# Performance work log

Measured on AMD Instinct MI355X. Metric: run time of the kernel, lower is better.

The kernel has to match this reference:

```python
import jax, jax.numpy as jnp
import numpy as np

N_S, N_T, E, B = 100000, 100000, 2000000, 10000
F_XS, F_XT, F_E, F_U = 10, 5, 10, 10


def setup_inputs() -> dict:
    key = jax.random.key(0)
    ks = jax.random.split(key, 8)
    return {
        "x_s": jax.random.normal(ks[0], (N_S, F_XS), dtype=jnp.float32),
        "x_t": jax.random.normal(ks[1], (N_T, F_XT), dtype=jnp.float32),
        "edge_index": jax.random.randint(ks[2], (2, E), 0, N_S),
        "edge_attr": jax.random.normal(ks[3], (E, F_E), dtype=jnp.float32),
        "u": jax.random.normal(ks[4], (B, F_U), dtype=jnp.float32),
        "batch_e": jax.random.randint(ks[5], (E,), 0, B),
        "W1": jax.random.normal(ks[6], (F_XS + F_XT + F_E + F_U, F_E), dtype=jnp.float32) * (1.0 / np.sqrt(F_XS + F_XT + F_E + F_U)),
        "b1": jnp.zeros((F_E,), dtype=jnp.float32),
        "W2": jax.random.normal(ks[7], (F_E, F_E), dtype=jnp.float32) * (1.0 / np.sqrt(F_E)),
        "b2": jnp.zeros((F_E,), dtype=jnp.float32),
    }


def reference(x_s, x_t, edge_index, edge_attr, u, batch_e, W1, b1, W2, b2):
    src, tgt = edge_index[0], edge_index[1]
    # Gather + concat: [E, F_xs + F_xt + F_e + F_u]
    h = jnp.concatenate([x_s[src], x_t[tgt], edge_attr, u[batch_e]], axis=-1)
    h = jax.nn.leaky_relu(h @ W1 + b1, negative_slope=0.1)
    return h @ W2 + b2  # [E, F_e]
```

## Files before the change

### kernel.cpp

```cpp
#include <hip/hip_runtime.h>


#define F_XS 10
#define F_XT 5
#define F_E  10
#define F_U  10
#define F_IN 35
#define BLOCK 256

typedef float vf4 __attribute__((ext_vector_type(4)));
typedef float vf2 __attribute__((ext_vector_type(2)));
typedef int   vi4 __attribute__((ext_vector_type(4)));
typedef _Float16 f16;

__global__ __launch_bounds__(256) void convert_tables_kernel(
    const float* __restrict__ xs, const float* __restrict__ xt, const float* __restrict__ uu,
    f16* __restrict__ xs_h, f16* __restrict__ xt_h, f16* __restrict__ u_h,
    int n_xs_elems, int n_u_elems, int n_t_rows)
{
    const int tid = blockIdx.x * blockDim.x + threadIdx.x;
    if (tid < n_xs_elems) {
        xs_h[tid] = (f16)xs[tid];
    } else if (tid < n_xs_elems + n_u_elems) {
        const int i = tid - n_xs_elems;
        u_h[i] = (f16)uu[i];
    } else {
        const int r = tid - n_xs_elems - n_u_elems;
        if (r < n_t_rows) {
            const float* p = xt + (long long)r * F_XT;
            f16* q = xt_h + (long long)r * 6;
            #pragma unroll
            for (int i = 0; i < 5; ++i) q[i] = (f16)p[i];
            q[5] = (f16)0.f;
        }
    }
}

__device__ __forceinline__ void compute_edge_attrfirst(
    const f16* __restrict__ s, const f16* __restrict__ t, const f16* __restrict__ uv,
    const float* __restrict__ a,
    const float* __restrict__ W1, const float* __restrict__ b1,
    const float* __restrict__ W2, const float* __restrict__ b2,
    float* __restrict__ o)
{
    float h[F_E];
    #pragma unroll
    for (int j = 0; j < F_E; ++j) h[j] = b1[j];

    #pragma unroll
    for (int k = 0; k < 10; ++k) {
        const float x = a[k];
        #pragma unroll
        for (int j = 0; j < F_E; ++j) h[j] = fmaf(x, W1[(15 + k) * F_E + j], h[j]);
    }
    #pragma unroll
    for (int k = 0; k < 10; ++k) {
        const float x = (float)s[k];
        #pragma unroll
        for (int j = 0; j < F_E; ++j) h[j] = fmaf(x, W1[k * F_E + j], h[j]);
    }
    #pragma unroll
    for (int k = 0; k < 5; ++k) {
        const float x = (float)t[k];
        #pragma unroll
        for (int j = 0; j < F_E; ++j) h[j] = fmaf(x, W1[(10 + k) * F_E + j], h[j]);
    }
    #pragma unroll
    for (int k = 0; k < 10; ++k) {
        const float x = (float)uv[k];
        #pragma unroll
        for (int j = 0; j < F_E; ++j) h[j] = fmaf(x, W1[(25 + k) * F_E + j], h[j]);
    }

    #pragma unroll
    for (int j = 0; j < F_E; ++j) h[j] = (h[j] >= 0.0f) ? h[j] : 0.1f * h[j];

    #pragma unroll
    for (int j = 0; j < F_E; ++j) o[j] = b2[j];
    #pragma unroll
    for (int k = 0; k < F_E; ++k) {
        const float x = h[k];
        #pragma unroll
        for (int j = 0; j < F_E; ++j) o[j] = fmaf(x, W2[k * F_E + j], o[j]);
    }
}

__global__ __launch_bounds__(256, 8) void edge_model_lds2_kernel(
    const f16*   __restrict__ xs_h,
    const f16*   __restrict__ xt_h,
    const int*   __restrict__ edge_index,
    const float* __restrict__ edge_attr,
    const f16*   __restrict__ u_h,
    const int*   __restrict__ batch_e,
    const float* __restrict__ W1,
    const float* __restrict__ b1,
    const float* __restrict__ W2,
    const float* __restrict__ b2,
    float*       __restrict__ out,
    int E)
{
    __shared__ __align__(16) int   idx_lds[3 * BLOCK];
    __shared__ __align__(16) float row_lds[10 * BLOCK];

    const int tid = threadIdx.x;
    const long long blockBase = (long long)blockIdx.x * BLOCK;

    if (blockBase + BLOCK <= E) {
        vi4 idxv;
        if (tid < 192) {
            const int* p;
            if (tid < 64)       p = edge_index + blockBase + 4 * tid;
            else if (tid < 128) p = edge_index + E + blockBase + 4 * (tid - 64);
            else                p = batch_e + blockBase + 4 * (tid - 128);
            idxv = __builtin_nontemporal_load((const vi4*)p);
        }

        const vf4* pa = (const vf4*)(edge_attr + blockBase * F_E);
        vf4 A0 = __builtin_nontemporal_load(pa + tid);
        vf4 A1 = __builtin_nontemporal_load(pa + tid + 256);
        vf4 A2;
        if (tid < 128) A2 = __builtin_nontemporal_load(pa + tid + 512);

        if (tid < 192) *(vi4*)(idx_lds + 4 * tid) = idxv;
        *(vf4*)(row_lds + 4 * tid)         = A0;
        *(vf4*)(row_lds + 4 * (tid + 256)) = A1;
        if (tid < 128) *(vf4*)(row_lds + 4 * (tid + 512)) = A2;
        __syncthreads();

        const int src = idx_lds[tid];
        const int tgt = idx_lds[256 + tid];
        const int be  = idx_lds[512 + tid];

        f16 s[10];  __builtin_memcpy(s,  xs_h + (long long)src * 10, 20);
        f16 tt[8];  __builtin_memcpy(tt, xt_h + (long long)tgt * 6, 16);
        f16 uv[10]; __builtin_memcpy(uv, u_h  + (long long)be  * 10, 20);

        float af[F_E];
        #pragma unroll
        for (int q = 0; q < 5; ++q) {
            const vf2 v = *(const vf2*)(row_lds + 10 * tid + 2 * q);
            af[2 * q]     = v.x;
            af[2 * q + 1] = v.y;
        }

        float o[F_E];
        compute_edge_attrfirst(s, tt, uv, af, W1, b1, W2, b2, o);

        #pragma unroll
        for (int q = 0; q < 5; ++q) {
            vf2 v; v.x = o[2 * q]; v.y = o[2 * q + 1];
            *(vf2*)(row_lds + 10 * tid + 2 * q) = v;
        }
        __syncthreads();

        float* po = out + blockBase * F_E;
        *(vf4*)(po + 4 * tid)         = *(const vf4*)(row_lds + 4 * tid);
        *(vf4*)(po + 4 * (tid + 256)) = *(const vf4*)(row_lds + 4 * (tid + 256));
        if (tid < 128)
            *(vf4*)(po + 4 * (tid + 512)) = *(const vf4*)(row_lds + 4 * (tid + 512));
    } else {
        const long long e = blockBase + tid;
        if (e < E) {
            const int src = edge_index[e];
            const int tgt = edge_index[E + e];
            const int be  = batch_e[e];
            f16 s1[10], t1[8], u1[10];
            __builtin_memcpy(s1, xs_h + (long long)src * 10, 20);
            __builtin_memcpy(t1, xt_h + (long long)tgt * 6, 16);
            __builtin_memcpy(u1, u_h  + (long long)be  * 10, 20);
            float a1[F_E];
            #pragma unroll
            for (int k = 0; k < F_E; ++k) a1[k] = edge_attr[e * F_E + k];
            float o1[F_E];
            compute_edge_attrfirst(s1, t1, u1, a1, W1, b1, W2, b2, o1);
            #pragma unroll
            for (int j = 0; j < F_E; ++j) out[e * F_E + j] = o1[j];
        }
    }
}

__global__ __launch_bounds__(256) void edge_model_f16tab_kernel(
    const f16*   __restrict__ xs_h, const f16* __restrict__ xt_h,
    const int*   __restrict__ edge_index, const float* __restrict__ edge_attr,
    const f16*   __restrict__ u_h, const int* __restrict__ batch_e,
    const float* __restrict__ W1, const float* __restrict__ b1,
    const float* __restrict__ W2, const float* __restrict__ b2,
    float* __restrict__ out, int E)
{
    const int e = blockIdx.x * blockDim.x + threadIdx.x;
    if (e >= E) return;

    const int src = __builtin_nontemporal_load(edge_index + e);
    const int tgt = __builtin_nontemporal_load(edge_index + E + e);
    const int be  = __builtin_nontemporal_load(batch_e + e);

    f16 s[10];  __builtin_memcpy(s, xs_h + (long long)src * 10, 20);
    f16 t[8];   __builtin_memcpy(t, xt_h + (long long)tgt * 6, 16);
    f16 uv[10]; __builtin_memcpy(uv, u_h + (long long)be * 10, 20);

    const float* pe = edge_attr + (long long)e * F_E;
    vf4 a0 = __builtin_nontemporal_load((const vf4*)(pe));
    vf4 a1 = __builtin_nontemporal_load((const vf4*)(pe + 4));
    vf2 a2 = __builtin_nontemporal_load((const vf2*)(pe + 8));
    float af[F_E] = {a0.x,a0.y,a0.z,a0.w, a1.x,a1.y,a1.z,a1.w, a2.x,a2.y};

    float o[F_E];
    compute_edge_attrfirst(s, t, uv, af, W1, b1, W2, b2, o);

    float* po = out + (long long)e * F_E;
    vf4 w0; w0.x=o[0]; w0.y=o[1]; w0.z=o[2]; w0.w=o[3];
    vf4 w1; w1.x=o[4]; w1.y=o[5]; w1.z=o[6]; w1.w=o[7];
    vf2 w2; w2.x=o[8]; w2.y=o[9];
    *(vf4*)(po)     = w0;
    *(vf4*)(po + 4) = w1;
    *(vf2*)(po + 8) = w2;
}

__global__ __launch_bounds__(256) void edge_model_f32_kernel(
    const float* __restrict__ x_s, const float* __restrict__ x_t,
    const int*   __restrict__ edge_index, const float* __restrict__ edge_attr,
    const float* __restrict__ u, const int* __restrict__ batch_e,
    const float* __restrict__ W1, const float* __restrict__ b1,
    const float* __restrict__ W2, const float* __restrict__ b2,
    float* __restrict__ out, int E)
{
    const int e = blockIdx.x * blockDim.x + threadIdx.x;
    if (e >= E) return;
    const int src = __builtin_nontemporal_load(edge_index + e);
    const int tgt = __builtin_nontemporal_load(edge_index + E + e);
    const int be  = __builtin_nontemporal_load(batch_e + e);

    float in[F_IN];
    __builtin_memcpy(in,      x_s + (long long)src * F_XS, 40);
    __builtin_memcpy(in + 10, x_t + (long long)tgt * F_XT, 20);
    const float* pe = edge_attr + (long long)e * F_E;
    vf4 a0 = __builtin_nontemporal_load((const vf4*)(pe));
    vf4 a1 = __builtin_nontemporal_load((const vf4*)(pe + 4));
    vf2 a2 = __builtin_nontemporal_load((const vf2*)(pe + 8));
    in[15]=a0.x; in[16]=a0.y; in[17]=a0.z; in[18]=a0.w;
    in[19]=a1.x; in[20]=a1.y; in[21]=a1.z; in[22]=a1.w;
    in[23]=a2.x; in[24]=a2.y;
    __builtin_memcpy(in + 25, u + (long long)be * F_U, 40);

    float h[F_E];
    #pragma unroll
    for (int j = 0; j < F_E; ++j) h[j] = b1[j];
    #pragma unroll
    for (int k = 0; k < F_IN; ++k) {
        const float a = in[k];
        #pragma unroll
        for (int j = 0; j < F_E; ++j) h[j] = fmaf(a, W1[k * F_E + j], h[j]);
    }
    #pragma unroll
    for (int j = 0; j < F_E; ++j) h[j] = (h[j] >= 0.0f) ? h[j] : 0.1f * h[j];

    float o[F_E];
    #pragma unroll
    for (int j = 0; j < F_E; ++j) o[j] = b2[j];
    #pragma unroll
    for (int k = 0; k < F_E; ++k) {
        const float a = h[k];
        #pragma unroll
        for (int j = 0; j < F_E; ++j) o[j] = fmaf(a, W2[k * F_E + j], o[j]);
    }
    float* po = out + (long long)e * F_E;
    vf4 w0; w0.x=o[0]; w0.y=o[1]; w0.z=o[2]; w0.w=o[3];
    vf4 w1; w1.x=o[4]; w1.y=o[5]; w1.z=o[6]; w1.w=o[7];
    vf2 w2; w2.x=o[8]; w2.y=o[9];
    *(vf4*)(po)     = w0;
    *(vf4*)(po + 4) = w1;
    *(vf2*)(po + 8) = w2;
}

extern "C" void kernel_launch(void* const* d_in, const int* in_sizes, int n_in,
                              void* d_out, int out_size, void* d_ws, size_t ws_size,
                              hipStream_t stream) {
    const float* x_s        = (const float*)d_in[0];
    const float* x_t        = (const float*)d_in[1];
    const int*   edge_index = (const int*)  d_in[2];
    const float* edge_attr  = (const float*)d_in[3];
    const float* u          = (const float*)d_in[4];
    const int*   batch_e    = (const int*)  d_in[5];
    const float* W1         = (const float*)d_in[6];
    const float* b1         = (const float*)d_in[7];
    const float* W2         = (const float*)d_in[8];
    const float* b2         = (const float*)d_in[9];
    float*       out        = (float*)d_out;

    const int E   = in_sizes[5];
    const int N_S = in_sizes[0] / F_XS;
    const int N_T = in_sizes[1] / F_XT;
    const int Bn  = in_sizes[4] / F_U;

    const size_t xs_bytes = (size_t)N_S * 10 * sizeof(f16);
    const size_t xs_off   = 0;
    const size_t xt_off   = (xs_off + xs_bytes + 15) & ~(size_t)15;
    const size_t xt_bytes = (size_t)N_T * 6 * sizeof(f16) + 16;
    const size_t u_off    = (xt_off + xt_bytes + 15) & ~(size_t)15;
    const size_t u_bytes  = (size_t)Bn * 10 * sizeof(f16);
    const size_t need     = u_off + u_bytes;

    const int block = BLOCK;

    if (ws_size >= need) {
        f16* xs_h = (f16*)((char*)d_ws + xs_off);
        f16* xt_h = (f16*)((char*)d_ws + xt_off);
        f16* u_h  = (f16*)((char*)d_ws + u_off);

        const int n_xs = N_S * 10, n_u = Bn * 10;
        const int conv_threads = n_xs + n_u + N_T;
        convert_tables_kernel<<<(conv_threads + block - 1) / block, block, 0, stream>>>(
            x_s, x_t, u, xs_h, xt_h, u_h, n_xs, n_u, N_T);

        const int grid_e = (E + block - 1) / block;
        if ((E & 3) == 0) {
            edge_model_lds2_kernel<<<grid_e, block, 0, stream>>>(
                xs_h, xt_h, edge_index, edge_attr, u_h, batch_e, W1, b1, W2, b2, out, E);
        } else {
            edge_model_f16tab_kernel<<<grid_e, block, 0, stream>>>(
                xs_h, xt_h, edge_index, edge_attr, u_h, batch_e, W1, b1, W2, b2, out, E);
        }
    } else {
        const int grid_e = (E + block - 1) / block;
        edge_model_f32_kernel<<<grid_e, block, 0, stream>>>(
            x_s, x_t, edge_index, edge_attr, u, batch_e, W1, b1, W2, b2, out, E);
    }
}
```

Measured before the change: 224.5 us.

## Make edge kernel wave-local, replacing block barriers with wave barriers

Each 64-lane wave now stages its own slice of indices and edge attributes in a private LDS region and synchronises with wave barriers instead of block-wide __syncthreads. The edge_attr LDS stores are moved after the table gathers are issued, which lets the gathers overlap the staging. The launch-bounds occupancy hint of 8 blocks per unit is dropped. The aim is to stop waves from stalling on each other at block barriers. The risk is relying on wave-level LDS ordering and possibly higher register use now that the occupancy hint is gone.

```diff
diff --git a/kernel.cpp b/kernel.cpp
--- a/kernel.cpp
+++ b/kernel.cpp
@@ -7,6 +7,7 @@
 #define F_U  10
 #define F_IN 35
 #define BLOCK 256
+#define WAVES 4
 
 typedef float vf4 __attribute__((ext_vector_type(4)));
 typedef float vf2 __attribute__((ext_vector_type(2)));
@@ -85,7 +86,7 @@
     }
 }
 
-__global__ __launch_bounds__(256, 8) void edge_model_lds2_kernel(
+__global__ __launch_bounds__(256) void edge_model_wave_kernel(
     const f16*   __restrict__ xs_h,
     const f16*   __restrict__ xt_h,
     const int*   __restrict__ edge_index,
@@ -99,46 +100,54 @@
     float*       __restrict__ out,
     int E)
 {
-    __shared__ __align__(16) int   idx_lds[3 * BLOCK];
-    __shared__ __align__(16) float row_lds[10 * BLOCK];
-
-    const int tid = threadIdx.x;
-    const long long blockBase = (long long)blockIdx.x * BLOCK;
-
-    if (blockBase + BLOCK <= E) {
+    __shared__ __align__(16) int   idxw[WAVES][192];
+    __shared__ __align__(16) float roww[WAVES][640];
+
+    const int tid  = threadIdx.x;
+    const int wid  = tid >> 6;
+    const int lane = tid & 63;
+    const long long wbase = (long long)blockIdx.x * BLOCK + (long long)wid * 64;
+    if (wbase >= E) return;
+
+    int*   iw = idxw[wid];
+    float* rw = roww[wid];
+
+    if (wbase + 64 <= E) {
         vi4 idxv;
-        if (tid < 192) {
+        if (lane < 48) {
             const int* p;
-            if (tid < 64)       p = edge_index + blockBase + 4 * tid;
-            else if (tid < 128) p = edge_index + E + blockBase + 4 * (tid - 64);
-            else                p = batch_e + blockBase + 4 * (tid - 128);
+            if (lane < 16)      p = edge_index + wbase + 4 * lane;
+            else if (lane < 32) p = edge_index + E + wbase + 4 * (lane - 16);
+            else                p = batch_e + wbase + 4 * (lane - 32);
             idxv = __builtin_nontemporal_load((const vi4*)p);
         }
 
-        const vf4* pa = (const vf4*)(edge_attr + blockBase * F_E);
-        vf4 A0 = __builtin_nontemporal_load(pa + tid);
-        vf4 A1 = __builtin_nontemporal_load(pa + tid + 256);
+        const vf4* pa = (const vf4*)(edge_attr + wbase * F_E);
+        vf4 A0 = __builtin_nontemporal_load(pa + lane);
+        vf4 A1 = __builtin_nontemporal_load(pa + lane + 64);
         vf4 A2;
-        if (tid < 128) A2 = __builtin_nontemporal_load(pa + tid + 512);
-
-        if (tid < 192) *(vi4*)(idx_lds + 4 * tid) = idxv;
-        *(vf4*)(row_lds + 4 * tid)         = A0;
-        *(vf4*)(row_lds + 4 * (tid + 256)) = A1;
-        if (tid < 128) *(vf4*)(row_lds + 4 * (tid + 512)) = A2;
-        __syncthreads();
-
-        const int src = idx_lds[tid];
-        const int tgt = idx_lds[256 + tid];
-        const int be  = idx_lds[512 + tid];
+        if (lane < 32) A2 = __builtin_nontemporal_load(pa + 128 + lane);
+
+        if (lane < 48) *(vi4*)(iw + 4 * lane) = idxv;
+        __builtin_amdgcn_wave_barrier();
+
+        const int src = iw[lane];
+        const int tgt = iw[64 + lane];
+        const int be  = iw[128 + lane];
 
         f16 s[10];  __builtin_memcpy(s,  xs_h + (long long)src * 10, 20);
         f16 tt[8];  __builtin_memcpy(tt, xt_h + (long long)tgt * 6, 16);
         f16 uv[10]; __builtin_memcpy(uv, u_h  + (long long)be  * 10, 20);
 
+        *(vf4*)(rw + 4 * lane)        = A0;
+        *(vf4*)(rw + 4 * (lane + 64)) = A1;
+        if (lane < 32) *(vf4*)(rw + 4 * (128 + lane)) = A2;
+        __builtin_amdgcn_wave_barrier();
+
         float af[F_E];
         #pragma unroll
         for (int q = 0; q < 5; ++q) {
-            const vf2 v = *(const vf2*)(row_lds + 10 * tid + 2 * q);
+            const vf2 v = *(const vf2*)(rw + 10 * lane + 2 * q);
             af[2 * q]     = v.x;
             af[2 * q + 1] = v.y;
         }
@@ -149,17 +158,17 @@
         #pragma unroll
         for (int q = 0; q < 5; ++q) {
             vf2 v; v.x = o[2 * q]; v.y = o[2 * q + 1];
-            *(vf2*)(row_lds + 10 * tid + 2 * q) = v;
-        }
-        __syncthreads();
-
-        float* po = out + blockBase * F_E;
-        *(vf4*)(po + 4 * tid)         = *(const vf4*)(row_lds + 4 * tid);
-        *(vf4*)(po + 4 * (tid + 256)) = *(const vf4*)(row_lds + 4 * (tid + 256));
-        if (tid < 128)
-            *(vf4*)(po + 4 * (tid + 512)) = *(const vf4*)(row_lds + 4 * (tid + 512));
+            *(vf2*)(rw + 10 * lane + 2 * q) = v;
+        }
+        __builtin_amdgcn_wave_barrier();
+
+        float* po = out + wbase * F_E;
+        *(vf4*)(po + 4 * lane)        = *(const vf4*)(rw + 4 * lane);
+        *(vf4*)(po + 4 * (lane + 64)) = *(const vf4*)(rw + 4 * (lane + 64));
+        if (lane < 32)
+            *(vf4*)(po + 4 * (128 + lane)) = *(const vf4*)(rw + 4 * (128 + lane));
     } else {
-        const long long e = blockBase + tid;
+        const long long e = wbase + lane;
         if (e < E) {
             const int src = edge_index[e];
             const int tgt = edge_index[E + e];
@@ -314,7 +323,7 @@
 
         const int grid_e = (E + block - 1) / block;
         if ((E & 3) == 0) {
-            edge_model_lds2_kernel<<<grid_e, block, 0, stream>>>(
+            edge_model_wave_kernel<<<grid_e, block, 0, stream>>>(
                 xs_h, xt_h, edge_index, edge_attr, u_h, batch_e, W1, b1, W2, b2, out, E);
         } else {
             edge_model_f16tab_kernel<<<grid_e, block, 0, stream>>>(
```

After: 215.2 us. 4.1% less time.
